# Kernel optimization log

Measured on AMD Instinct MI355X. Metric: run time of the kernel, lower is better.

The kernel has to match this reference:

```python
import jax, jax.numpy as jnp
import numpy as np

V = 32000   # vocab_size
T = 2048    # train_len (pos embed table size)
E = 1024    # embed_dim
H = 16      # num_heads
FF = 4096   # ff_dim
L = 4       # num_layers
B, C = 2, 1024
D = E // H  # head_dim = 64
EPS = 1e-5


def setup_inputs() -> dict:
    key = jax.random.key(0)
    ks = jax.random.split(key, 12)
    s = 0.02
    inp = {
        "x": jax.random.randint(ks[0], (B, C), 0, V),
        "embed": jax.random.normal(ks[1], (V, E), jnp.float32) * s,
        "pos_embed": jax.random.normal(ks[2], (T, E), jnp.float32) * s,
        "Wq": jax.random.normal(ks[3], (L, E, E), jnp.float32) * s,
        "Wk": jax.random.normal(ks[4], (L, E, E), jnp.float32) * s,
        "Wv": jax.random.normal(ks[5], (L, E, E), jnp.float32) * s,
        "Wo": jax.random.normal(ks[6], (L, E, E), jnp.float32) * s,
        "ln1_w": jnp.ones((L, E), jnp.float32),
        "ln1_b": jnp.zeros((L, E), jnp.float32),
        "ln2_w": jnp.ones((L, E), jnp.float32),
        "ln2_b": jnp.zeros((L, E), jnp.float32),
        "W1": jax.random.normal(ks[7], (L, E, FF), jnp.float32) * s,
        "b1": jnp.zeros((L, FF), jnp.float32),
        "W2": jax.random.normal(ks[8], (L, FF, E), jnp.float32) * s,
        "b2": jnp.zeros((L, E), jnp.float32),
        "lnf_w": jnp.ones((E,), jnp.float32),
        "lnf_b": jnp.zeros((E,), jnp.float32),
        "Wout": jax.random.normal(ks[9], (E, V), jnp.float32) * s,
        "bout": jnp.zeros((V,), jnp.float32),
    }
    return inp


def _layernorm(h, w, b):
    mu = jnp.mean(h, axis=-1, keepdims=True)
    var = jnp.var(h, axis=-1, keepdims=True)
    return (h - mu) * jax.lax.rsqrt(var + EPS) * w + b


def reference(x, embed, pos_embed, Wq, Wk, Wv, Wo, ln1_w, ln1_b, ln2_w, ln2_b,
              W1, b1, W2, b2, lnf_w, lnf_b, Wout, bout):
    Bx, Cx = x.shape
    positions = jnp.clip(jnp.arange(Cx), 0, T - 1)  # 'clamp' extrapolation
    h = embed[x] + pos_embed[positions]             # [B,C,E]
    # causal mask: -inf above the diagonal
    mask = jnp.where(jnp.tril(jnp.ones((Cx, Cx), bool)), 0.0, -jnp.inf).astype(h.dtype)
    scale = 1.0 / np.sqrt(D)
    for i in range(L):
        hn = _layernorm(h, ln1_w[i], ln1_b[i])
        Q = (hn @ Wq[i]).reshape(Bx, Cx, H, D).transpose(0, 2, 1, 3)  # [B,H,C,D]
        K = (hn @ Wk[i]).reshape(Bx, Cx, H, D).transpose(0, 2, 1, 3)
        Vv = (hn @ Wv[i]).reshape(Bx, Cx, H, D).transpose(0, 2, 1, 3)
        scores = jnp.einsum('bhqd,bhkd->bhqk', Q, K) * scale + mask
        weights = jax.nn.softmax(scores, axis=-1)
        attn = jnp.einsum('bhqk,bhkd->bhqd', weights, Vv)
        attn = attn.transpose(0, 2, 1, 3).reshape(Bx, Cx, E) @ Wo[i]
        h = h + attn
        hn2 = _layernorm(h, ln2_w[i], ln2_b[i])
        h = h + jax.nn.gelu(hn2 @ W1[i] + b1[i], approximate=False) @ W2[i] + b2[i]
    return _layernorm(h, lnf_w, lnf_b) @ Wout + bout  # [B,C,V]
```

## Files before the change

kernel.cpp:

```cpp
#include <hip/hip_runtime.h>
#include <hip/hip_bf16.h>
#include <math.h>

constexpr int V  = 32000;
constexpr int E  = 1024;
constexpr int H  = 16;
constexpr int FF = 4096;
constexpr int L  = 4;
constexpr int B  = 2;
constexpr int C  = 1024;
constexpr int D  = 64;
constexpr int N  = B * C;
constexpr int E3 = 3 * E;
constexpr float EPS = 1e-5f;

typedef __hip_bfloat16 bf16;
typedef __bf16 bf16x8 __attribute__((ext_vector_type(8)));
typedef __bf16 bf16x4 __attribute__((ext_vector_type(4)));
typedef float  f32x4  __attribute__((ext_vector_type(4)));

#define AS1 __attribute__((address_space(1)))
#define AS3 __attribute__((address_space(3)))

__device__ inline bf16x8 lds_load8(const bf16* p) {
    bf16x4 lo = *(const bf16x4*)p;
    bf16x4 hi = *(const bf16x4*)(p + 4);
    bf16x8 r;
    r[0]=lo[0]; r[1]=lo[1]; r[2]=lo[2]; r[3]=lo[3];
    r[4]=hi[0]; r[5]=hi[1]; r[6]=hi[2]; r[7]=hi[3];
    return r;
}
__device__ inline void lds_store8(bf16* p, bf16x8 v) {
    bf16x4 lo, hi;
    lo[0]=v[0]; lo[1]=v[1]; lo[2]=v[2]; lo[3]=v[3];
    hi[0]=v[4]; hi[1]=v[5]; hi[2]=v[6]; hi[3]=v[7];
    *(bf16x4*)p = lo; *(bf16x4*)(p + 4) = hi;
}

__device__ inline bf16x8 lds_frag32(const bf16* sbase, int row, int c) {
    return *(const bf16x8*)(sbase + row * 32 + ((c ^ ((row >> 1) & 3)) << 3));
}
__device__ inline bf16x8 lds_frag64(const bf16* sbase, int row, int c) {
    return *(const bf16x8*)(sbase + row * 64 + ((c ^ (row & 7)) << 3));
}

__global__ void embed_ln_kernel(const int* __restrict__ x,
                                const float* __restrict__ embed,
                                const float* __restrict__ pos,
                                const float* __restrict__ w,
                                const float* __restrict__ b,
                                float* __restrict__ h,
                                bf16* __restrict__ hn) {
    __shared__ float red[256];
    int token = blockIdx.x;
    int tid = threadIdx.x;
    int c = token % C;
    int id = x[token];
    float4 ev = ((const float4*)(embed + (size_t)id * E))[tid];
    float4 pv = ((const float4*)(pos + (size_t)c * E))[tid];
    float4 xv;
    xv.x = ev.x + pv.x; xv.y = ev.y + pv.y;
    xv.z = ev.z + pv.z; xv.w = ev.w + pv.w;
    ((float4*)(h + (size_t)token * E))[tid] = xv;

    red[tid] = xv.x + xv.y + xv.z + xv.w;
    __syncthreads();
    for (int st = 128; st > 0; st >>= 1) {
        if (tid < st) red[tid] += red[tid + st];
        __syncthreads();
    }
    float mu = red[0] * (1.0f / E);
    __syncthreads();

    float d0 = xv.x - mu, d1 = xv.y - mu, d2 = xv.z - mu, d3 = xv.w - mu;
    red[tid] = d0 * d0 + d1 * d1 + d2 * d2 + d3 * d3;
    __syncthreads();
    for (int st = 128; st > 0; st >>= 1) {
        if (tid < st) red[tid] += red[tid + st];
        __syncthreads();
    }
    float var = red[0] * (1.0f / E);
    float inv = rsqrtf(var + EPS);

    float4 wv = ((const float4*)w)[tid];
    float4 bv = ((const float4*)b)[tid];
    float y0 = d0 * inv * wv.x + bv.x;
    float y1 = d1 * inv * wv.y + bv.y;
    float y2 = d2 * inv * wv.z + bv.z;
    float y3 = d3 * inv * wv.w + bv.w;
    ushort4 o;
    { bf16 t0 = __float2bfloat16(y0); o.x = *(ushort*)&t0; }
    { bf16 t1 = __float2bfloat16(y1); o.y = *(ushort*)&t1; }
    { bf16 t2 = __float2bfloat16(y2); o.z = *(ushort*)&t2; }
    { bf16 t3 = __float2bfloat16(y3); o.w = *(ushort*)&t3; }
    ((ushort4*)(hn + (size_t)token * E))[tid] = o;
}

__global__ void layernorm_kernel(const float* __restrict__ in,
                                 const float* __restrict__ w,
                                 const float* __restrict__ b,
                                 bf16* __restrict__ out) {
    __shared__ float red[256];
    int token = blockIdx.x;
    int tid = threadIdx.x;
    float4 xv = ((const float4*)(in + (size_t)token * E))[tid];

    red[tid] = xv.x + xv.y + xv.z + xv.w;
    __syncthreads();
    for (int st = 128; st > 0; st >>= 1) {
        if (tid < st) red[tid] += red[tid + st];
        __syncthreads();
    }
    float mu = red[0] * (1.0f / E);
    __syncthreads();

    float d0 = xv.x - mu, d1 = xv.y - mu, d2 = xv.z - mu, d3 = xv.w - mu;
    red[tid] = d0 * d0 + d1 * d1 + d2 * d2 + d3 * d3;
    __syncthreads();
    for (int st = 128; st > 0; st >>= 1) {
        if (tid < st) red[tid] += red[tid + st];
        __syncthreads();
    }
    float var = red[0] * (1.0f / E);
    float inv = rsqrtf(var + EPS);

    float4 wv = ((const float4*)w)[tid];
    float4 bv = ((const float4*)b)[tid];
    float y0 = d0 * inv * wv.x + bv.x;
    float y1 = d1 * inv * wv.y + bv.y;
    float y2 = d2 * inv * wv.z + bv.z;
    float y3 = d3 * inv * wv.w + bv.w;
    ushort4 o;
    { bf16 t0 = __float2bfloat16(y0); o.x = *(ushort*)&t0; }
    { bf16 t1 = __float2bfloat16(y1); o.y = *(ushort*)&t1; }
    { bf16 t2 = __float2bfloat16(y2); o.z = *(ushort*)&t2; }
    { bf16 t3 = __float2bfloat16(y3); o.w = *(ushort*)&t3; }
    ((ushort4*)(out + (size_t)token * E))[tid] = o;
}

__global__ void transpose_all(const float* __restrict__ Wq,
                              const float* __restrict__ Wk,
                              const float* __restrict__ Wv,
                              const float* __restrict__ Wo,
                              const float* __restrict__ W1,
                              const float* __restrict__ W2,
                              const float* __restrict__ Wout,
                              bf16* __restrict__ qkvt, bf16* __restrict__ wot,
                              bf16* __restrict__ w1t,  bf16* __restrict__ w2t,
                              bf16* __restrict__ wvt) {
    __shared__ float tile[64][65];
    int b = blockIdx.x;
    const float* src; bf16* dst;
    int Nn, Kk, n0, k0;
    if (b >= 12288) {
        int rem = b - 12288;
        src = Wout; dst = wvt; Nn = V; Kk = E;
        n0 = (rem % 500) * 64; k0 = (rem / 500) * 64;
    } else {
        int i = b / 3072, r = b % 3072;
        if (r < 1024) {
            int mat = r >> 8, rr = r & 255;
            n0 = (rr & 15) * 64; k0 = (rr >> 4) * 64;
            Nn = E; Kk = E;
            const float* srcs[4] = {Wq, Wk, Wv, Wo};
            src = srcs[mat] + (size_t)i * E * E;
            dst = (mat < 3) ? qkvt + ((size_t)i * E3 + (size_t)mat * E) * E
                            : wot + (size_t)i * E * E;
        } else if (r < 2048) {
            int rr = r - 1024;
            n0 = (rr & 63) * 64; k0 = (rr >> 6) * 64;
            Nn = FF; Kk = E;
            src = W1 + (size_t)i * E * FF;
            dst = w1t + (size_t)i * FF * E;
        } else {
            int rr = r - 2048;
            n0 = (rr & 15) * 64; k0 = (rr >> 4) * 64;
            Nn = E; Kk = FF;
            src = W2 + (size_t)i * FF * E;
            dst = w2t + (size_t)i * E * FF;
        }
    }
    int tid = threadIdx.x;
    #pragma unroll
    for (int it = 0; it < 4; ++it) {
        int idx = it * 256 + tid;
        int row = idx >> 4, c4 = (idx & 15) * 4;
        *(float4*)&tile[row][c4] =
            *(const float4*)&src[(size_t)(k0 + row) * Nn + n0 + c4];
    }
    __syncthreads();
    #pragma unroll
    for (int it = 0; it < 2; ++it) {
        int s = it * 256 + tid;
        int nrow = s >> 3, kc = s & 7;
        bf16x8 v;
        #pragma unroll
        for (int j = 0; j < 8; ++j)
            v[j] = (__bf16)__float2bfloat16(tile[kc * 8 + j][nrow]);
        *(bf16x8*)&dst[(size_t)(n0 + nrow) * Kk + k0 + kc * 8] = v;
    }
}

__global__ void transpose_v(const bf16* __restrict__ qkv,
                            bf16* __restrict__ vt) {
    __shared__ ushort tile[32][34];
    int c0 = blockIdx.x * 32;
    int d0 = (blockIdx.y & 1) * 32;
    int bh = blockIdx.y >> 1;
    int bb = bh >> 4, hh = bh & 15;
    int tx = threadIdx.x & 31, ty = threadIdx.x >> 5;
    const ushort* src = (const ushort*)qkv;
    ushort* dst = (ushort*)vt;
    #pragma unroll
    for (int i = 0; i < 32; i += 8)
        tile[ty + i][tx] = src[(size_t)(bb * C + c0 + ty + i) * E3 + 2 * E + hh * D + d0 + tx];
    __syncthreads();
    #pragma unroll
    for (int i = 0; i < 32; i += 8)
        dst[((size_t)bh * D + d0 + ty + i) * C + c0 + tx] = tile[tx][ty + i];
}

__launch_bounds__(512, 2)
__global__ void gemm_v8(const bf16* __restrict__ A,
                        const bf16* __restrict__ Bt,
                        const float* __restrict__ bias,
                        float* __restrict__ outF,
                        int M, int Nc, int K) {
    __shared__ __align__(16) bf16 sA[2][2][128 * 64];
    __shared__ __align__(16) bf16 sB[2][2][128 * 64];

    int tid  = threadIdx.x;
    int lane = tid & 63;
    int wid  = tid >> 6;
    int wm   = wid >> 2;
    int wn   = wid & 3;
    int l16  = lane & 15;
    int lhi  = lane >> 4;

    int nwg = gridDim.x * gridDim.y;
    int id  = blockIdx.y * gridDim.x + blockIdx.x;
    int cpx = nwg >> 3;
    int swz = (id & 7) * cpx + (id >> 3);
    int bx  = swz / gridDim.y;
    int by  = swz % gridDim.y;

    size_t brow = (size_t)by * 256;
    size_t bcol = (size_t)bx * 256;

    f32x4 acc[8][4] = {};

    auto stageA = [&](int buf, int half, int t) {
        size_t k0 = (size_t)t * 64;
        #pragma unroll
        for (int j = 0; j < 2; ++j) {
            int s = j * 512 + tid;
            int row = s >> 3;
            int ch  = (s & 7) ^ (row & 7);
            int ldso = (j * 512 + wid * 64) * 8;
            const bf16* g = A + (brow + half * 128 + row) * K + k0 + ch * 8;
            __builtin_amdgcn_global_load_lds(
                (const AS1 void*)g, (AS3 void*)(&sA[buf][half][0] + ldso), 16, 0, 0);
        }
    };
    auto stageB = [&](int buf, int half, int t) {
        size_t k0 = (size_t)t * 64;
        #pragma unroll
        for (int j = 0; j < 2; ++j) {
            int s = j * 512 + tid;
            int row = s >> 3;
            int ch  = (s & 7) ^ (row & 7);
            int ldso = (j * 512 + wid * 64) * 8;
            const bf16* g = Bt + (bcol + half * 128 + row) * K + k0 + ch * 8;
            __builtin_amdgcn_global_load_lds(
                (const AS1 void*)g, (AS3 void*)(&sB[buf][half][0] + ldso), 16, 0, 0);
        }
    };

    int NT = K / 64;
    stageA(0, 0, 0); stageB(0, 0, 0);
    stageB(0, 1, 0); stageA(0, 1, 0);
    stageA(1, 0, 1); stageB(1, 0, 1);

    bf16x8 ra[4][2], rb[2][2], rb0[2][2];

    for (int t = 0; t < NT; ++t) {
        int cur = t & 1, nxt = cur ^ 1;

        if (t == NT - 1) asm volatile("s_waitcnt vmcnt(4)" ::: "memory");
        else             asm volatile("s_waitcnt vmcnt(8)" ::: "memory");
        __builtin_amdgcn_sched_barrier(0);
        __builtin_amdgcn_s_barrier();
        if (t + 1 < NT) { stageB(nxt, 1, t + 1); stageA(nxt, 1, t + 1); }
        #pragma unroll
        for (int m = 0; m < 4; ++m)
            #pragma unroll
            for (int kh = 0; kh < 2; ++kh)
                ra[m][kh] = lds_frag64(&sA[cur][0][0], wm * 64 + m * 16 + l16, kh * 4 + lhi);
        #pragma unroll
        for (int n = 0; n < 2; ++n)
            #pragma unroll
            for (int kh = 0; kh < 2; ++kh)
                rb0[n][kh] = lds_frag64(&sB[cur][0][0], wn * 32 + n * 16 + l16, kh * 4 + lhi);
        __builtin_amdgcn_s_setprio(1);
        #pragma unroll
        for (int m = 0; m < 4; ++m)
            #pragma unroll
            for (int n = 0; n < 2; ++n)
                #pragma unroll
                for (int kh = 0; kh < 2; ++kh)
                    acc[m][n] = __builtin_amdgcn_mfma_f32_16x16x32_bf16(
                        ra[m][kh], rb0[n][kh], acc[m][n], 0, 0, 0);
        __builtin_amdgcn_s_setprio(0);

        if (t == NT - 1) asm volatile("s_waitcnt vmcnt(0)" ::: "memory");
        else             asm volatile("s_waitcnt vmcnt(8)" ::: "memory");
        __builtin_amdgcn_sched_barrier(0);
        __builtin_amdgcn_s_barrier();
        #pragma unroll
        for (int n = 0; n < 2; ++n)
            #pragma unroll
            for (int kh = 0; kh < 2; ++kh)
                rb[n][kh] = lds_frag64(&sB[cur][1][0], wn * 32 + n * 16 + l16, kh * 4 + lhi);
        __builtin_amdgcn_s_setprio(1);
        #pragma unroll
        for (int m = 0; m < 4; ++m)
            #pragma unroll
            for (int n = 0; n < 2; ++n)
                #pragma unroll
                for (int kh = 0; kh < 2; ++kh)
                    acc[m][n + 2] = __builtin_amdgcn_mfma_f32_16x16x32_bf16(
                        ra[m][kh], rb[n][kh], acc[m][n + 2], 0, 0, 0);
        __builtin_amdgcn_s_setprio(0);

        if (t + 2 < NT) { stageA(cur, 0, t + 2); stageB(cur, 0, t + 2); }
        #pragma unroll
        for (int m = 0; m < 4; ++m)
            #pragma unroll
            for (int kh = 0; kh < 2; ++kh)
                ra[m][kh] = lds_frag64(&sA[cur][1][0], wm * 64 + m * 16 + l16, kh * 4 + lhi);
        __builtin_amdgcn_s_setprio(1);
        #pragma unroll
        for (int m = 0; m < 4; ++m)
            #pragma unroll
            for (int n = 0; n < 2; ++n)
                #pragma unroll
                for (int kh = 0; kh < 2; ++kh)
                    acc[m + 4][n + 2] = __builtin_amdgcn_mfma_f32_16x16x32_bf16(
                        ra[m][kh], rb[n][kh], acc[m + 4][n + 2], 0, 0, 0);
        __builtin_amdgcn_s_setprio(0);

        __builtin_amdgcn_s_setprio(1);
        #pragma unroll
        for (int m = 0; m < 4; ++m)
            #pragma unroll
            for (int n = 0; n < 2; ++n)
                #pragma unroll
                for (int kh = 0; kh < 2; ++kh)
                    acc[m + 4][n] = __builtin_amdgcn_mfma_f32_16x16x32_bf16(
                        ra[m][kh], rb0[n][kh], acc[m + 4][n], 0, 0, 0);
        __builtin_amdgcn_s_setprio(0);
    }

    int crow = lhi * 4;
    #pragma unroll
    for (int qm = 0; qm < 2; ++qm)
        #pragma unroll
        for (int qn = 0; qn < 2; ++qn)
            #pragma unroll
            for (int m = 0; m < 4; ++m)
                #pragma unroll
                for (int n = 0; n < 2; ++n)
                    #pragma unroll
                    for (int r = 0; r < 4; ++r) {
                        size_t row = brow + qm * 128 + wm * 64 + m * 16 + crow + r;
                        size_t col = bcol + qn * 128 + wn * 32 + n * 16 + l16;
                        float val = acc[qm * 4 + m][qn * 2 + n][r];
                        val += bias[col];
                        outF[row * Nc + col] = val;
                    }
}

__launch_bounds__(256, 2)
__global__ void gemm_bf16_128(const bf16* __restrict__ A,
                              const bf16* __restrict__ Bt,
                              const float* __restrict__ bias,
                              const float* __restrict__ res,
                              float* __restrict__ outF,
                              bf16*  __restrict__ outB,
                              int M, int Nc, int K, int gelu_flag) {
    __shared__ __align__(16) bf16 sA[4][128 * 32];
    __shared__ __align__(16) bf16 sB[4][128 * 32];

    int tid  = threadIdx.x;
    int lane = tid & 63;
    int wid  = tid >> 6;
    int wr   = wid >> 1;
    int wc   = wid & 1;
    int l16  = lane & 15;
    int lhi  = lane >> 4;

    int nwg = gridDim.x * gridDim.y;
    int id  = blockIdx.y * gridDim.x + blockIdx.x;
    int cpx = nwg >> 3;
    int swz = (id & 7) * cpx + (id >> 3);
    int bx  = swz / gridDim.y;
    int by  = swz % gridDim.y;

    size_t brow = (size_t)by * 128;
    size_t bcol = (size_t)bx * 128;

    f32x4 acc[4][4] = {};

    auto stage = [&](int buf, int t) {
        size_t k0 = (size_t)t * 32;
        #pragma unroll
        for (int j = 0; j < 2; ++j) {
            int s = j * 256 + tid;
            int row = s >> 2;
            int ch  = (s & 3) ^ ((row >> 1) & 3);
            int ldso = (j * 256 + wid * 64) * 8;
            const bf16* ga = A + (brow + row) * K + k0 + ch * 8;
            __builtin_amdgcn_global_load_lds(
                (const AS1 void*)ga, (AS3 void*)(&sA[buf][0] + ldso), 16, 0, 0);
        }
        #pragma unroll
        for (int j = 0; j < 2; ++j) {
            int s = j * 256 + tid;
            int row = s >> 2;
            int ch  = (s & 3) ^ ((row >> 1) & 3);
            int ldso = (j * 256 + wid * 64) * 8;
            const bf16* gb = Bt + (bcol + row) * K + k0 + ch * 8;
            __builtin_amdgcn_global_load_lds(
                (const AS1 void*)gb, (AS3 void*)(&sB[buf][0] + ldso), 16, 0, 0);
        }
    };

    int NT = K / 32;
    stage(0, 0);
    stage(1, 1);

    for (int t = 0; t < NT; ++t) {
        if (t + 2 < NT) {
            stage((t + 2) & 3, t + 2);
            asm volatile("s_waitcnt vmcnt(8)" ::: "memory");
        } else if (t + 1 < NT) {
            asm volatile("s_waitcnt vmcnt(4)" ::: "memory");
        } else {
            asm volatile("s_waitcnt vmcnt(0)" ::: "memory");
        }
        __builtin_amdgcn_sched_barrier(0);
        __builtin_amdgcn_s_barrier();

        const bf16* As_ = &sA[t & 3][0];
        const bf16* Bs_ = &sB[t & 3][0];
        bf16x8 ra[4], rb[4];
        #pragma unroll
        for (int m = 0; m < 4; ++m)
            ra[m] = lds_frag32(As_, wr * 64 + m * 16 + l16, lhi);
        #pragma unroll
        for (int n = 0; n < 4; ++n)
            rb[n] = lds_frag32(Bs_, wc * 64 + n * 16 + l16, lhi);

        __builtin_amdgcn_s_setprio(1);
        #pragma unroll
        for (int m = 0; m < 4; ++m)
            #pragma unroll
            for (int n = 0; n < 4; ++n)
                acc[m][n] = __builtin_amdgcn_mfma_f32_16x16x32_bf16(
                    ra[m], rb[n], acc[m][n], 0, 0, 0);
        __builtin_amdgcn_s_setprio(0);
    }

    int crow = lhi * 4;
    #pragma unroll
    for (int m = 0; m < 4; ++m) {
        #pragma unroll
        for (int n = 0; n < 4; ++n) {
            #pragma unroll
            for (int r = 0; r < 4; ++r) {
                size_t row = brow + wr * 64 + m * 16 + crow + r;
                size_t col = bcol + wc * 64 + n * 16 + l16;
                float val = acc[m][n][r];
                if (bias) val += bias[col];
                if (gelu_flag) val = 0.5f * val * (1.0f + erff(val * 0.70710678118f));
                if (res) val += res[row * Nc + col];
                if (outF) outF[row * Nc + col] = val;
                if (outB) outB[row * Nc + col] = __float2bfloat16(val);
            }
        }
    }
}

__launch_bounds__(256, 2)
__global__ void gemm_bf16_64(const bf16* __restrict__ A,
                             const bf16* __restrict__ Bt,
                             const float* __restrict__ bias,
                             const float* __restrict__ res,
                             float* __restrict__ outF,
                             bf16*  __restrict__ outB,
                             int M, int Nc, int K, int gelu_flag) {
    __shared__ __align__(16) bf16 sA[3][64 * 64];
    __shared__ __align__(16) bf16 sB[3][128 * 64];

    int tid  = threadIdx.x;
    int lane = tid & 63;
    int wid  = tid >> 6;
    int l16  = lane & 15;
    int lhi  = lane >> 4;

    int nwg = gridDim.x * gridDim.y;
    int id  = blockIdx.y * gridDim.x + blockIdx.x;
    int cpx = nwg >> 3;
    int swz = (id & 7) * cpx + (id >> 3);
    int bx  = swz / gridDim.y;
    int by  = swz % gridDim.y;

    size_t brow = (size_t)by * 64;
    size_t bcol = (size_t)bx * 128;

    f32x4 acc[4][2] = {};

    auto stage = [&](int buf, int t) {
        size_t k0 = (size_t)t * 64;
        #pragma unroll
        for (int j = 0; j < 2; ++j) {
            int s = j * 256 + tid;
            int row = s >> 3;
            int ch  = (s & 7) ^ (row & 7);
            int ldso = (j * 256 + wid * 64) * 8;
            const bf16* ga = A + (brow + row) * K + k0 + ch * 8;
            __builtin_amdgcn_global_load_lds(
                (const AS1 void*)ga, (AS3 void*)(&sA[buf][0] + ldso), 16, 0, 0);
        }
        #pragma unroll
        for (int j = 0; j < 4; ++j) {
            int s = j * 256 + tid;
            int row = s >> 3;
            int ch  = (s & 7) ^ (row & 7);
            int ldso = (j * 256 + wid * 64) * 8;
            const bf16* gb = Bt + (bcol + row) * K + k0 + ch * 8;
            __builtin_amdgcn_global_load_lds(
                (const AS1 void*)gb, (AS3 void*)(&sB[buf][0] + ldso), 16, 0, 0);
        }
    };

    int NT = K / 64;
    stage(0, 0); stage(1, 1);
    int cur = 0, sl2 = 2;

    for (int t = 0; t < NT; ++t) {
        if (t == NT - 1) asm volatile("s_waitcnt vmcnt(0)" ::: "memory");
        else             asm volatile("s_waitcnt vmcnt(6)" ::: "memory");
        __builtin_amdgcn_sched_barrier(0);
        __builtin_amdgcn_s_barrier();
        if (t + 2 < NT) stage(sl2, t + 2);

        const bf16* As_ = &sA[cur][0];
        const bf16* Bs_ = &sB[cur][0];
        bf16x8 ra[4][2], rb[2][2];
        #pragma unroll
        for (int m = 0; m < 4; ++m)
            #pragma unroll
            for (int kh = 0; kh < 2; ++kh)
                ra[m][kh] = lds_frag64(As_, m * 16 + l16, kh * 4 + lhi);
        #pragma unroll
        for (int n = 0; n < 2; ++n)
            #pragma unroll
            for (int kh = 0; kh < 2; ++kh)
                rb[n][kh] = lds_frag64(Bs_, wid * 32 + n * 16 + l16, kh * 4 + lhi);

        __builtin_amdgcn_s_setprio(1);
        #pragma unroll
        for (int m = 0; m < 4; ++m)
            #pragma unroll
            for (int n = 0; n < 2; ++n)
                #pragma unroll
                for (int kh = 0; kh < 2; ++kh)
                    acc[m][n] = __builtin_amdgcn_mfma_f32_16x16x32_bf16(
                        ra[m][kh], rb[n][kh], acc[m][n], 0, 0, 0);
        __builtin_amdgcn_s_setprio(0);

        cur = (cur == 2) ? 0 : cur + 1;
        sl2 = (sl2 == 2) ? 0 : sl2 + 1;
    }

    int crow = lhi * 4;
    #pragma unroll
    for (int m = 0; m < 4; ++m) {
        #pragma unroll
        for (int n = 0; n < 2; ++n) {
            #pragma unroll
            for (int r = 0; r < 4; ++r) {
                size_t row = brow + m * 16 + crow + r;
                size_t col = bcol + wid * 32 + n * 16 + l16;
                float val = acc[m][n][r];
                if (bias) val += bias[col];
                if (gelu_flag) val = 0.5f * val * (1.0f + erff(val * 0.70710678118f));
                if (res) val += res[row * Nc + col];
                if (outF) outF[row * Nc + col] = val;
                if (outB) outB[row * Nc + col] = __float2bfloat16(val);
            }
        }
    }
}

constexpr int QBLK = 64;
constexpr int KVB  = 64;
constexpr int PSTR = 72;

__launch_bounds__(256)
__global__ void flash_attn(const bf16* __restrict__ qkv,
                           const bf16* __restrict__ vt,
                           bf16* __restrict__ O) {
    __shared__ bf16 sK[KVB][PSTR];
    __shared__ bf16 sV[D][PSTR];
    __shared__ bf16 sP[4][16][PSTR];

    int qt = blockIdx.x;
    int bh = blockIdx.y;
    if (bh & 1) qt = (C / QBLK - 1) - qt;
    int bb = bh >> 4, hh = bh & 15;
    int qbase = qt * QBLK;
    int tid = threadIdx.x, lane = tid & 63, w = tid >> 6;
    int l16 = lane & 15, lhi = lane >> 4;

    int qrow = qbase + w * 16 + l16;
    const bf16* qp = qkv + (size_t)(bb * C + qrow) * E3 + hh * D + lhi * 8;
    bf16x8 qf0 = *(const bf16x8*)qp;
    bf16x8 qf1 = *(const bf16x8*)(qp + 32);

    f32x4 oa[4] = {};
    float m_run[4] = {-INFINITY, -INFINITY, -INFINITY, -INFINITY};
    float l_run[4] = {0.f, 0.f, 0.f, 0.f};

    int NTk = qt + 1;
    int srow = tid >> 3, sc8 = tid & 7;
    int srow2 = srow + 32;

    bf16x8 kvR0, kvR1, vvR0, vvR1;
    kvR0 = *(const bf16x8*)(qkv + (size_t)(bb * C + srow)  * E3 + E + hh * D + sc8 * 8);
    kvR1 = *(const bf16x8*)(qkv + (size_t)(bb * C + srow2) * E3 + E + hh * D + sc8 * 8);
    vvR0 = *(const bf16x8*)(vt + ((size_t)bh * D + srow)  * C + sc8 * 8);
    vvR1 = *(const bf16x8*)(vt + ((size_t)bh * D + srow2) * C + sc8 * 8);

    for (int t = 0; t < NTk; ++t) {
        __syncthreads();
        lds_store8(&sK[srow][sc8 * 8],  kvR0);
        lds_store8(&sK[srow2][sc8 * 8], kvR1);
        lds_store8(&sV[srow][sc8 * 8],  vvR0);
        lds_store8(&sV[srow2][sc8 * 8], vvR1);

        bf16x8 kvN0, kvN1, vvN0, vvN1;
        if (t + 1 < NTk) {
            int k0n = (t + 1) * KVB;
            kvN0 = *(const bf16x8*)(qkv + (size_t)(bb * C + k0n + srow)  * E3 + E + hh * D + sc8 * 8);
            kvN1 = *(const bf16x8*)(qkv + (size_t)(bb * C + k0n + srow2) * E3 + E + hh * D + sc8 * 8);
            vvN0 = *(const bf16x8*)(vt + ((size_t)bh * D + srow)  * C + k0n + sc8 * 8);
            vvN1 = *(const bf16x8*)(vt + ((size_t)bh * D + srow2) * C + k0n + sc8 * 8);
        }
        __syncthreads();

        int k0 = t * KVB;
        f32x4 sc[4] = {};
        #pragma unroll
        for (int n = 0; n < 4; ++n) {
            bf16x8 kf0 = lds_load8(&sK[n * 16 + l16][lhi * 8]);
            sc[n] = __builtin_amdgcn_mfma_f32_16x16x32_bf16(qf0, kf0, sc[n], 0, 0, 0);
            bf16x8 kf1 = lds_load8(&sK[n * 16 + l16][32 + lhi * 8]);
            sc[n] = __builtin_amdgcn_mfma_f32_16x16x32_bf16(qf1, kf1, sc[n], 0, 0, 0);
        }

        int qg = qbase + w * 16 + lhi * 4;
        #pragma unroll
        for (int n = 0; n < 4; ++n) {
            int kg = k0 + n * 16 + l16;
            #pragma unroll
            for (int r = 0; r < 4; ++r) {
                float vvv = sc[n][r] * 0.125f;
                if (t == qt && kg > qg + r) vvv = -1e30f;
                sc[n][r] = vvv;
            }
        }

        float pm[4];
        #pragma unroll
        for (int r = 0; r < 4; ++r)
            pm[r] = fmaxf(fmaxf(sc[0][r], sc[1][r]), fmaxf(sc[2][r], sc[3][r]));
        #pragma unroll
        for (int xm = 1; xm <= 8; xm <<= 1)
            #pragma unroll
            for (int r = 0; r < 4; ++r)
                pm[r] = fmaxf(pm[r], __shfl_xor(pm[r], xm));

        float corr[4];
        #pragma unroll
        for (int r = 0; r < 4; ++r) {
            float mn = fmaxf(m_run[r], pm[r]);
            corr[r] = __expf(m_run[r] - mn);
            m_run[r] = mn;
        }
        f32x4 p[4];
        #pragma unroll
        for (int n = 0; n < 4; ++n)
            #pragma unroll
            for (int r = 0; r < 4; ++r)
                p[n][r] = __expf(sc[n][r] - m_run[r]);

        float rsum[4];
        #pragma unroll
        for (int r = 0; r < 4; ++r)
            rsum[r] = p[0][r] + p[1][r] + p[2][r] + p[3][r];
        #pragma unroll
        for (int xm = 1; xm <= 8; xm <<= 1)
            #pragma unroll
            for (int r = 0; r < 4; ++r)
                rsum[r] += __shfl_xor(rsum[r], xm);
        #pragma unroll
        for (int r = 0; r < 4; ++r)
            l_run[r] = l_run[r] * corr[r] + rsum[r];
        #pragma unroll
        for (int nd = 0; nd < 4; ++nd)
            #pragma unroll
            for (int r = 0; r < 4; ++r)
                oa[nd][r] *= corr[r];

        #pragma unroll
        for (int n = 0; n < 4; ++n)
            #pragma unroll
            for (int r = 0; r < 4; ++r)
                sP[w][lhi * 4 + r][n * 16 + l16] = __float2bfloat16(p[n][r]);
        bf16x8 pa0 = lds_load8(&sP[w][l16][lhi * 8]);
        bf16x8 pa1 = lds_load8(&sP[w][l16][32 + lhi * 8]);

        #pragma unroll
        for (int nd = 0; nd < 4; ++nd) {
            bf16x8 vf0 = lds_load8(&sV[nd * 16 + l16][lhi * 8]);
            oa[nd] = __builtin_amdgcn_mfma_f32_16x16x32_bf16(pa0, vf0, oa[nd], 0, 0, 0);
            bf16x8 vf1 = lds_load8(&sV[nd * 16 + l16][32 + lhi * 8]);
            oa[nd] = __builtin_amdgcn_mfma_f32_16x16x32_bf16(pa1, vf1, oa[nd], 0, 0, 0);
        }

        if (t + 1 < NTk) { kvR0 = kvN0; kvR1 = kvN1; vvR0 = vvN0; vvR1 = vvN1; }
    }

    #pragma unroll
    for (int r = 0; r < 4; ++r) {
        float inv = 1.0f / l_run[r];
        int qg = qbase + w * 16 + lhi * 4 + r;
        bf16* orow = O + (size_t)(bb * C + qg) * E + hh * D;
        #pragma unroll
        for (int nd = 0; nd < 4; ++nd)
            orow[nd * 16 + l16] = __float2bfloat16(oa[nd][r] * inv);
    }
}

extern "C" void kernel_launch(void* const* d_in, const int* in_sizes, int n_in,
                              void* d_out, int out_size, void* d_ws, size_t ws_size,
                              hipStream_t stream) {
    const int*   x     = (const int*)  d_in[0];
    const float* embed = (const float*)d_in[1];
    const float* pos   = (const float*)d_in[2];
    const float* Wq    = (const float*)d_in[3];
    const float* Wk    = (const float*)d_in[4];
    const float* Wv    = (const float*)d_in[5];
    const float* Wo    = (const float*)d_in[6];
    const float* ln1w  = (const float*)d_in[7];
    const float* ln1b  = (const float*)d_in[8];
    const float* ln2w  = (const float*)d_in[9];
    const float* ln2b  = (const float*)d_in[10];
    const float* W1    = (const float*)d_in[11];
    const float* b1    = (const float*)d_in[12];
    const float* W2    = (const float*)d_in[13];
    const float* b2    = (const float*)d_in[14];
    const float* lnfw  = (const float*)d_in[15];
    const float* lnfb  = (const float*)d_in[16];
    const float* Wout  = (const float*)d_in[17];
    const float* bout  = (const float*)d_in[18];
    float* out = (float*)d_out;

    char* p = (char*)d_ws;
    auto alloc = [&](size_t bytes) {
        char* r = p;
        p += (bytes + 255) & ~(size_t)255;
        return r;
    };
    float* h    = (float*)alloc((size_t)N * E  * 4);
    bf16*  qkvb = (bf16*) alloc((size_t)N * E3 * 2);
    bf16*  hn   = (bf16*) alloc((size_t)N * E  * 2);
    bf16*  attn = (bf16*) alloc((size_t)N * E  * 2);
    bf16*  ff   = (bf16*) alloc((size_t)N * FF * 2);
    bf16*  vt   = (bf16*) alloc((size_t)B * H * D * C * 2);
    bf16*  qkvt = (bf16*) alloc((size_t)L * E3 * E * 2);
    bf16*  wot  = (bf16*) alloc((size_t)L * E  * E * 2);
    bf16*  w1t  = (bf16*) alloc((size_t)L * FF * E * 2);
    bf16*  w2t  = (bf16*) alloc((size_t)L * E  * FF * 2);
    bf16*  wvt  = (bf16*) alloc((size_t)V * E  * 2 + 4096);

    transpose_all<<<20288, 256, 0, stream>>>(Wq, Wk, Wv, Wo, W1, W2, Wout,
                                             qkvt, wot, w1t, w2t, wvt);

    embed_ln_kernel<<<N, 256, 0, stream>>>(x, embed, pos, ln1w, ln1b, h, hn);

    dim3 gQKV(E3 / 128, N / 128);
    dim3 gF  (FF / 128, N / 128);
    dim3 gV  (V  / 256, N / 256);
    dim3 gO  (E  / 128, N / 64);

    for (int i = 0; i < L; ++i) {
        if (i > 0)
            layernorm_kernel<<<N, 256, 0, stream>>>(h, ln1w + i * E, ln1b + i * E, hn);

        gemm_bf16_128<<<gQKV, 256, 0, stream>>>(hn, qkvt + (size_t)i * E3 * E,
                                                nullptr, nullptr, nullptr, qkvb,
                                                N, E3, E, 0);

        transpose_v<<<dim3(C / 32, 2 * B * H), 256, 0, stream>>>(qkvb, vt);

        flash_attn<<<dim3(C / QBLK, B * H), 256, 0, stream>>>(qkvb, vt, attn);

        gemm_bf16_64<<<gO, 256, 0, stream>>>(attn, wot + (size_t)i * E * E,
                                             nullptr, h, h, nullptr,
                                             N, E, E, 0);

        layernorm_kernel<<<N, 256, 0, stream>>>(h, ln2w + i * E, ln2b + i * E, hn);

        gemm_bf16_128<<<gF, 256, 0, stream>>>(hn, w1t + (size_t)i * FF * E,
                                              b1 + (size_t)i * FF, nullptr,
                                              nullptr, ff,
                                              N, FF, E, 1);
        gemm_bf16_64<<<gO, 256, 0, stream>>>(ff, w2t + (size_t)i * E * FF,
                                             b2 + (size_t)i * E, h, h, nullptr,
                                             N, E, FF, 0);
    }

    layernorm_kernel<<<N, 256, 0, stream>>>(h, lnfw, lnfb, hn);
    gemm_v8<<<gV, 512, 0, stream>>>(hn, wvt, bout, out, N, V, E);
}
```

Baseline: 1.223 ms.

## Fuse V transpose into flash attention via swizzled LDS scatter

Drops the separate transpose_v kernel and its scratch buffer. Flash attention now reads V rows straight from the QKV buffer and transposes them while writing to shared memory, using an XOR swizzle on the column index to limit bank conflicts. The reads in the PV product apply the matching swizzle. This saves one launch per layer and a round trip through global memory, at the cost of scalar 2-byte LDS stores in the attention inner loop.

```diff
diff --git a/kernel.cpp b/kernel.cpp
--- a/kernel.cpp
+++ b/kernel.cpp
@@ -201,25 +201,6 @@
     }
 }
 
-__global__ void transpose_v(const bf16* __restrict__ qkv,
-                            bf16* __restrict__ vt) {
-    __shared__ ushort tile[32][34];
-    int c0 = blockIdx.x * 32;
-    int d0 = (blockIdx.y & 1) * 32;
-    int bh = blockIdx.y >> 1;
-    int bb = bh >> 4, hh = bh & 15;
-    int tx = threadIdx.x & 31, ty = threadIdx.x >> 5;
-    const ushort* src = (const ushort*)qkv;
-    ushort* dst = (ushort*)vt;
-    #pragma unroll
-    for (int i = 0; i < 32; i += 8)
-        tile[ty + i][tx] = src[(size_t)(bb * C + c0 + ty + i) * E3 + 2 * E + hh * D + d0 + tx];
-    __syncthreads();
-    #pragma unroll
-    for (int i = 0; i < 32; i += 8)
-        dst[((size_t)bh * D + d0 + ty + i) * C + c0 + tx] = tile[tx][ty + i];
-}
-
 __launch_bounds__(512, 2)
 __global__ void gemm_v8(const bf16* __restrict__ A,
                         const bf16* __restrict__ Bt,
@@ -610,7 +591,6 @@
 
 __launch_bounds__(256)
 __global__ void flash_attn(const bf16* __restrict__ qkv,
-                           const bf16* __restrict__ vt,
                            bf16* __restrict__ O) {
     __shared__ bf16 sK[KVB][PSTR];
     __shared__ bf16 sV[D][PSTR];
@@ -636,27 +616,32 @@
     int NTk = qt + 1;
     int srow = tid >> 3, sc8 = tid & 7;
     int srow2 = srow + 32;
+    int c1 = srow  ^ (sc8 << 3);
+    int c2 = srow2 ^ (sc8 << 3);
 
     bf16x8 kvR0, kvR1, vvR0, vvR1;
     kvR0 = *(const bf16x8*)(qkv + (size_t)(bb * C + srow)  * E3 + E + hh * D + sc8 * 8);
     kvR1 = *(const bf16x8*)(qkv + (size_t)(bb * C + srow2) * E3 + E + hh * D + sc8 * 8);
-    vvR0 = *(const bf16x8*)(vt + ((size_t)bh * D + srow)  * C + sc8 * 8);
-    vvR1 = *(const bf16x8*)(vt + ((size_t)bh * D + srow2) * C + sc8 * 8);
+    vvR0 = *(const bf16x8*)(qkv + (size_t)(bb * C + srow)  * E3 + 2 * E + hh * D + sc8 * 8);
+    vvR1 = *(const bf16x8*)(qkv + (size_t)(bb * C + srow2) * E3 + 2 * E + hh * D + sc8 * 8);
 
     for (int t = 0; t < NTk; ++t) {
         __syncthreads();
         lds_store8(&sK[srow][sc8 * 8],  kvR0);
         lds_store8(&sK[srow2][sc8 * 8], kvR1);
-        lds_store8(&sV[srow][sc8 * 8],  vvR0);
-        lds_store8(&sV[srow2][sc8 * 8], vvR1);
+        #pragma unroll
+        for (int j = 0; j < 8; ++j) {
+            *((__bf16*)&sV[sc8 * 8 + j][c1]) = vvR0[j];
+            *((__bf16*)&sV[sc8 * 8 + j][c2]) = vvR1[j];
+        }
 
         bf16x8 kvN0, kvN1, vvN0, vvN1;
         if (t + 1 < NTk) {
             int k0n = (t + 1) * KVB;
             kvN0 = *(const bf16x8*)(qkv + (size_t)(bb * C + k0n + srow)  * E3 + E + hh * D + sc8 * 8);
             kvN1 = *(const bf16x8*)(qkv + (size_t)(bb * C + k0n + srow2) * E3 + E + hh * D + sc8 * 8);
-            vvN0 = *(const bf16x8*)(vt + ((size_t)bh * D + srow)  * C + k0n + sc8 * 8);
-            vvN1 = *(const bf16x8*)(vt + ((size_t)bh * D + srow2) * C + k0n + sc8 * 8);
+            vvN0 = *(const bf16x8*)(qkv + (size_t)(bb * C + k0n + srow)  * E3 + 2 * E + hh * D + sc8 * 8);
+            vvN1 = *(const bf16x8*)(qkv + (size_t)(bb * C + k0n + srow2) * E3 + 2 * E + hh * D + sc8 * 8);
         }
         __syncthreads();
 
@@ -734,9 +719,11 @@
 
         #pragma unroll
         for (int nd = 0; nd < 4; ++nd) {
-            bf16x8 vf0 = lds_load8(&sV[nd * 16 + l16][lhi * 8]);
+            int d0 = nd * 16 + l16;
+            int dsw = ((nd * 2 + (l16 >> 3)) & 7) << 3;
+            bf16x8 vf0 = lds_load8(&sV[d0][(lhi * 8) ^ dsw]);
             oa[nd] = __builtin_amdgcn_mfma_f32_16x16x32_bf16(pa0, vf0, oa[nd], 0, 0, 0);
-            bf16x8 vf1 = lds_load8(&sV[nd * 16 + l16][32 + lhi * 8]);
+            bf16x8 vf1 = lds_load8(&sV[d0][(32 + lhi * 8) ^ dsw]);
             oa[nd] = __builtin_amdgcn_mfma_f32_16x16x32_bf16(pa1, vf1, oa[nd], 0, 0, 0);
         }
 
@@ -789,7 +776,6 @@
     bf16*  hn   = (bf16*) alloc((size_t)N * E  * 2);
     bf16*  attn = (bf16*) alloc((size_t)N * E  * 2);
     bf16*  ff   = (bf16*) alloc((size_t)N * FF * 2);
-    bf16*  vt   = (bf16*) alloc((size_t)B * H * D * C * 2);
     bf16*  qkvt = (bf16*) alloc((size_t)L * E3 * E * 2);
     bf16*  wot  = (bf16*) alloc((size_t)L * E  * E * 2);
     bf16*  w1t  = (bf16*) alloc((size_t)L * FF * E * 2);
@@ -814,9 +800,7 @@
                                                 nullptr, nullptr, nullptr, qkvb,
                                                 N, E3, E, 0);
 
-        transpose_v<<<dim3(C / 32, 2 * B * H), 256, 0, stream>>>(qkvb, vt);
-
-        flash_attn<<<dim3(C / QBLK, B * H), 256, 0, stream>>>(qkvb, vt, attn);
+        flash_attn<<<dim3(C / QBLK, B * H), 256, 0, stream>>>(qkvb, attn);
 
         gemm_bf16_64<<<gO, 256, 0, stream>>>(attn, wot + (size_t)i * E * E,
                                              nullptr, h, h, nullptr,
```

Result: no change. 1.220 ms, median of 2 (-0.3%).
